# Kernel optimization log

Hardware: AMD Instinct MI355X
Metric: run time of the kernel (lower is better)

## Reference

```python
import jax, jax.numpy as jnp
import numpy as np

SCALE = 4.0
GRID = 64
B, T, A, C = 4, 256, 3, 13
F = 5 + C  # x,y,z,r,conf,cls...


def setup_inputs() -> dict:
    key = jax.random.key(0)
    k1, k2, k3, k4, k5 = jax.random.split(key, 5)
    p = jax.random.normal(k1, (B, A, GRID, GRID, GRID, F), dtype=jnp.float32)
    xyz = jax.random.uniform(k2, (B, T, 3), minval=4.0, maxval=SCALE * GRID - 4.0)
    r = jax.random.uniform(k3, (B, T, 1), minval=6.0, maxval=20.0)
    conf = (jax.random.uniform(k4, (B, T, 1)) < 0.6).astype(jnp.float32)
    cls = jax.nn.one_hot(jax.random.randint(k5, (B, T), 0, C), C, dtype=jnp.float32)
    targets = jnp.concatenate([xyz, r, conf, cls], axis=-1)  # [B,T,18]
    anchor = jnp.array([[[8.0], [12.0], [16.0]]], dtype=jnp.float32)  # [1,A,1]
    return {"p": p, "targets": targets, "anchor": anchor}


def _bce(logits, t):
    # BCEWithLogitsLoss (pos_weight=1), elementwise
    return t * jax.nn.softplus(-logits) + (1.0 - t) * jax.nn.softplus(logits)


def _eiou(box1, box2, eps=1e-7):
    # boxes are (x,y,z,r): axis-aligned cubes of side r centered at xyz (3D EIoU)
    c1, r1 = box1[:, :3], box1[:, 3]
    c2, r2 = box2[:, :3], box2[:, 3]
    h1, h2 = r1[:, None] * 0.5, r2[:, None] * 0.5
    lo = jnp.maximum(c1 - h1, c2 - h2)
    hi = jnp.minimum(c1 + h1, c2 + h2)
    inter = jnp.prod(jnp.clip(hi - lo, 0.0), axis=-1)
    union = r1 ** 3 + r2 ** 3 - inter + eps
    iou = inter / union
    clo = jnp.minimum(c1 - h1, c2 - h2)
    chi = jnp.maximum(c1 + h1, c2 + h2)
    cdim = chi - clo  # enclosing box per-axis extent
    rho2 = jnp.sum((c1 - c2) ** 2, axis=-1)
    c2diag = jnp.sum(cdim ** 2, axis=-1) + eps
    size_pen = jnp.sum(((r1 - r2) ** 2)[:, None] / (cdim ** 2 + eps), axis=-1)
    return iou - rho2 / c2diag - size_pen


def reference(p, targets, anchor):
    Bs, An, K, J, I, Fd = p.shape
    Cn = Fd - 5
    g, gr = 0.5, 0.0
    Tn = targets.shape[1]
    n = Bs * Tn
    x = targets.reshape(n, Fd)
    b0 = jnp.repeat(jnp.arange(Bs), Tn)
    conf_m = x[:, 4] > 0.5
    anchor_norm = anchor[0] / SCALE  # [A,1]
    gxyzr = x[:, :4] / SCALE
    rn = gxyzr[:, 3]
    ratio = rn[None, :] / anchor_norm  # [A,n]
    aok = jnp.maximum(ratio, 1.0 / ratio) < 4.0
    gxyz = gxyzr[:, :3]
    gdim = jnp.array([K, J, I], dtype=p.dtype)  # gain[1:]
    gxyz_i = gdim - gxyz
    m1 = (gxyz % 1.0 < g) & (gxyz > 1.0)
    m2 = (gxyz_i % 1.0 < g) & (gxyz_i > 1.0)
    fm = jnp.stack([jnp.ones_like(m1[:, 0]), m1[:, 0], m1[:, 1], m1[:, 2], m2[:, 0], m2[:, 1], m2[:, 2]])  # [7,n]
    off = jnp.array([[0, 0, 0], [1, 0, 0], [0, 1, 0], [0, 0, 1], [-1, 0, 0], [0, -1, 0], [0, 0, -1]], dtype=p.dtype) * g
    valid = (conf_m[None, None, :] & aok[None, :, :] & fm[:, None, :]).reshape(-1)  # [7*A*n]
    bidx = jnp.broadcast_to(b0[None, None, :], (7, An, n)).reshape(-1)
    aidx = jnp.broadcast_to(jnp.arange(An)[None, :, None], (7, An, n)).reshape(-1)
    gxyz_c = jnp.broadcast_to(gxyz[None, None], (7, An, n, 3))
    off_c = jnp.broadcast_to(off[:, None, None, :], (7, An, n, 3))
    gijk_f = jnp.trunc(jax.lax.stop_gradient(gxyz_c - off_c))  # torch .long() truncates
    gijk = gijk_f.astype(jnp.int32).reshape(-1, 3)
    gi = jnp.clip(gijk[:, 0], 0, I - 1)
    gj = jnp.clip(gijk[:, 1], 0, J - 1)
    gk = jnp.clip(gijk[:, 2], 0, K - 1)
    tbox = jnp.concatenate([(gxyz_c - gijk_f).reshape(-1, 3), jnp.broadcast_to(rn[None, None, :], (7, An, n)).reshape(-1, 1)], axis=1)
    anchors = anchor_norm[aidx]  # [N,1]
    tcls = jnp.broadcast_to(x[None, None, :, 5:], (7, An, n, Cn)).reshape(-1, Cn)
    pred = p[bidx, aidx, gk, gj, gi]  # [N,F]
    pxyz = jax.nn.sigmoid(pred[:, :3]) * 2.0 - 0.5
    pr = (jax.nn.sigmoid(pred[:, 3:4]) * 2.0) ** 2 * anchors
    pbox = jnp.concatenate([pxyz, pr], axis=1)
    ei = _eiou(pbox, tbox)
    w = valid.astype(p.dtype)
    nv = jnp.maximum(jnp.sum(w), 1.0)
    loss_bbox = jnp.sum(w * (1.0 - ei)) / nv  # masked mean == torch mean over filtered rows
    iou_d = jax.lax.stop_gradient(jnp.clip(ei, 0.0))
    objv = (1.0 - gr) + gr * iou_d  # gr=0 -> 1.0
    tobj = jnp.zeros((Bs, An, K, J, I), dtype=p.dtype).at[bidx, aidx, gk, gj, gi].max(w * objv)
    loss_cls = jnp.sum(w[:, None] * _bce(pred[:, 5:], tcls)) / (nv * Cn)
    loss_obj = jnp.mean(_bce(p[..., 4], tobj))
    lb = loss_bbox * 1.0
    lo = loss_obj * 20.0
    lc = loss_cls * 10.0
    return ((lb + lo + lc) * Bs, lo, lc)
```

## Files before the change

### kernel.cpp

```cpp
#include <hip/hip_runtime.h>
#include <math.h>

#define NTGT   1024
#define NCAND  (21 * NTGT)
#define NCELL  (4 * 3 * 64 * 64 * 64)
#define BITW   (NCELL / 32)

__device__ __forceinline__ float softplusf(float x) {
    return fmaxf(x, 0.0f) + log1pf(__expf(-fabsf(x)));
}
__device__ __forceinline__ float sigmoidf(float x) {
    return 1.0f / (1.0f + __expf(-x));
}

__global__ __launch_bounds__(256) void cand_kernel(
    const float* __restrict__ p, const float* __restrict__ tg,
    const float* __restrict__ anchor, float* __restrict__ acc,
    unsigned int* __restrict__ bitmap)
{
    int idx = blockIdx.x * 256 + threadIdx.x;
    float nv_v = 0.f, bb_v = 0.f, cl_v = 0.f;
    if (idx < NCAND) {
        int t  = idx & (NTGT - 1);
        int oa = idx >> 10;
        int a  = oa % 3;
        int o  = oa / 3;
        const float* x = tg + t * 18;
        float conf = x[4];
        float rn   = x[3] * 0.25f;
        float an   = anchor[a] * 0.25f;
        float ratio = rn / an;
        bool ok = (conf > 0.5f) && (fmaxf(ratio, 1.0f / ratio) < 4.0f);
        float gv[3] = { x[0] * 0.25f, x[1] * 0.25f, x[2] * 0.25f };
        float off[3] = { 0.f, 0.f, 0.f };
        if (o >= 1) {
            if (o <= 3) {
                int c = o - 1;
                float v = gv[c];
                ok = ok && ((v - floorf(v)) < 0.5f) && (v > 1.0f);
                off[c] = 0.5f;
            } else {
                int c = o - 4;
                float vi = 64.0f - gv[c];
                ok = ok && ((vi - floorf(vi)) < 0.5f) && (vi > 1.0f);
                off[c] = -0.5f;
            }
        }
        if (ok) {
            float tb[3]; int gq[3];
            #pragma unroll
            for (int c = 0; c < 3; c++) {
                float f = truncf(gv[c] - off[c]);
                tb[c] = gv[c] - f;
                int ii = (int)f;
                gq[c] = min(max(ii, 0), 63);
            }
            int b0 = t >> 8;
            unsigned int cell =
                ((((unsigned)(b0 * 3 + a) * 64u + (unsigned)gq[2]) * 64u
                  + (unsigned)gq[1]) * 64u) + (unsigned)gq[0];
            const float* pp = p + (size_t)cell * 18u;
            float pd[18];
            #pragma unroll
            for (int f = 0; f < 18; f++) pd[f] = pp[f];

            float c1[3];
            #pragma unroll
            for (int c = 0; c < 3; c++) c1[c] = sigmoidf(pd[c]) * 2.0f - 0.5f;
            float s4 = sigmoidf(pd[3]) * 2.0f;
            float r1 = s4 * s4 * an;
            float r2 = rn;

            float h1 = 0.5f * r1, h2 = 0.5f * r2;
            float inter = 1.f, rho2 = 0.f, c2d = 0.f, spen = 0.f;
            float dr2 = (r1 - r2) * (r1 - r2);
            #pragma unroll
            for (int c = 0; c < 3; c++) {
                float lo1 = c1[c] - h1, hi1 = c1[c] + h1;
                float lo2 = tb[c] - h2, hi2 = tb[c] + h2;
                inter *= fmaxf(fminf(hi1, hi2) - fmaxf(lo1, lo2), 0.f);
                float cd  = fmaxf(hi1, hi2) - fminf(lo1, lo2);
                float cd2 = cd * cd;
                float d   = c1[c] - tb[c];
                rho2 += d * d;
                c2d  += cd2;
                spen += dr2 / (cd2 + 1e-7f);
            }
            float uni = r1 * r1 * r1 + r2 * r2 * r2 - inter + 1e-7f;
            float ei  = inter / uni - rho2 / (c2d + 1e-7f) - spen;

            nv_v = 1.0f;
            bb_v = 1.0f - ei;
            float cl = 0.f;
            #pragma unroll
            for (int c = 0; c < 13; c++) {
                float l = pd[5 + c];
                cl += softplusf(l) - x[5 + c] * l;
            }
            cl_v = cl;
            atomicOr(&bitmap[cell >> 5], 1u << (cell & 31u));
        }
    }
    #pragma unroll
    for (int s = 32; s > 0; s >>= 1) {
        nv_v += __shfl_down(nv_v, s, 64);
        bb_v += __shfl_down(bb_v, s, 64);
        cl_v += __shfl_down(cl_v, s, 64);
    }
    if ((threadIdx.x & 63) == 0 && nv_v != 0.f) {
        atomicAdd(&acc[0], nv_v);
        atomicAdd(&acc[1], bb_v);
        atomicAdd(&acc[2], cl_v);
    }
}

__global__ __launch_bounds__(256) void obj_kernel(
    const float* __restrict__ p, const unsigned int* __restrict__ bitmap,
    float* __restrict__ acc)
{
    int stride = gridDim.x * blockDim.x;
    float s = 0.f;
    for (int i = blockIdx.x * blockDim.x + threadIdx.x; i < NCELL; i += stride) {
        float l = p[(size_t)i * 18u + 4u];
        unsigned int bit = (bitmap[i >> 5] >> (i & 31)) & 1u;
        s += softplusf(l) - (bit ? l : 0.f);
    }
    #pragma unroll
    for (int sh = 32; sh > 0; sh >>= 1) s += __shfl_down(s, sh, 64);
    __shared__ float sm[4];
    int lane = threadIdx.x & 63, w = threadIdx.x >> 6;
    if (lane == 0) sm[w] = s;
    __syncthreads();
    if (threadIdx.x == 0) {
        atomicAdd(&acc[3], sm[0] + sm[1] + sm[2] + sm[3]);
    }
}

__global__ void final_kernel(const float* __restrict__ acc, float* __restrict__ out)
{
    float nv = fmaxf(acc[0], 1.0f);
    float lb = acc[1] / nv;
    float lc = acc[2] / (nv * 13.0f) * 10.0f;
    float lo = acc[3] * (20.0f / (float)NCELL);
    out[0] = (lb + lo + lc) * 4.0f;
    out[1] = lo;
    out[2] = lc;
}

extern "C" void kernel_launch(void* const* d_in, const int* in_sizes, int n_in,
                              void* d_out, int out_size, void* d_ws, size_t ws_size,
                              hipStream_t stream) {
    const float* p       = (const float*)d_in[0];
    const float* targets = (const float*)d_in[1];
    const float* anchor  = (const float*)d_in[2];
    float* out = (float*)d_out;

    float* acc = (float*)d_ws;
    unsigned int* bitmap = (unsigned int*)((char*)d_ws + 16);

    hipMemsetAsync(d_ws, 0, 16 + (size_t)BITW * 4, stream);

    cand_kernel<<<NCAND / 256, 256, 0, stream>>>(p, targets, anchor, acc, bitmap);
    obj_kernel<<<3072, 256, 0, stream>>>(p, bitmap, acc);
    final_kernel<<<1, 1, 0, stream>>>(acc, out);
}
```

Measured before the change: 330.1 us.

## Fuse candidate and objectness kernels by subtracting unique positive logits

Measured after the change: 311.0 us. 1.06x faster.

```diff
diff --git a/kernel.cpp b/kernel.cpp
--- a/kernel.cpp
+++ b/kernel.cpp
@@ -3,127 +3,130 @@
 
 #define NTGT   1024
 #define NCAND  (21 * NTGT)
+#define NCBLK  (NCAND / 256)
 #define NCELL  (4 * 3 * 64 * 64 * 64)
 #define BITW   (NCELL / 32)
+#define NBLK   2048
 
 __device__ __forceinline__ float softplusf(float x) {
-    return fmaxf(x, 0.0f) + log1pf(__expf(-fabsf(x)));
+    return fmaxf(x, 0.0f) + __logf(1.0f + __expf(-fabsf(x)));
 }
 __device__ __forceinline__ float sigmoidf(float x) {
     return 1.0f / (1.0f + __expf(-x));
 }
 
-__global__ __launch_bounds__(256) void cand_kernel(
+__global__ __launch_bounds__(256) void fused_kernel(
     const float* __restrict__ p, const float* __restrict__ tg,
     const float* __restrict__ anchor, float* __restrict__ acc,
     unsigned int* __restrict__ bitmap)
 {
-    int idx = blockIdx.x * 256 + threadIdx.x;
-    float nv_v = 0.f, bb_v = 0.f, cl_v = 0.f;
-    if (idx < NCAND) {
-        int t  = idx & (NTGT - 1);
-        int oa = idx >> 10;
-        int a  = oa % 3;
-        int o  = oa / 3;
-        const float* x = tg + t * 18;
-        float conf = x[4];
-        float rn   = x[3] * 0.25f;
-        float an   = anchor[a] * 0.25f;
-        float ratio = rn / an;
-        bool ok = (conf > 0.5f) && (fmaxf(ratio, 1.0f / ratio) < 4.0f);
-        float gv[3] = { x[0] * 0.25f, x[1] * 0.25f, x[2] * 0.25f };
-        float off[3] = { 0.f, 0.f, 0.f };
-        if (o >= 1) {
-            if (o <= 3) {
-                int c = o - 1;
-                float v = gv[c];
-                ok = ok && ((v - floorf(v)) < 0.5f) && (v > 1.0f);
-                off[c] = 0.5f;
-            } else {
-                int c = o - 4;
-                float vi = 64.0f - gv[c];
-                ok = ok && ((vi - floorf(vi)) < 0.5f) && (vi > 1.0f);
-                off[c] = -0.5f;
+    if (blockIdx.x < NCBLK) {
+        int idx = blockIdx.x * 256 + threadIdx.x;
+        float nv_v = 0.f, bb_v = 0.f, cl_v = 0.f, ob_v = 0.f;
+        {
+            int t  = idx & (NTGT - 1);
+            int oa = idx >> 10;
+            int a  = oa % 3;
+            int o  = oa / 3;
+            const float* x = tg + t * 18;
+            float conf = x[4];
+            float rn   = x[3] * 0.25f;
+            float an   = anchor[a] * 0.25f;
+            float ratio = rn / an;
+            bool ok = (conf > 0.5f) && (fmaxf(ratio, 1.0f / ratio) < 4.0f);
+            float gv[3] = { x[0] * 0.25f, x[1] * 0.25f, x[2] * 0.25f };
+            float off[3] = { 0.f, 0.f, 0.f };
+            if (o >= 1) {
+                if (o <= 3) {
+                    int c = o - 1;
+                    float v = gv[c];
+                    ok = ok && ((v - floorf(v)) < 0.5f) && (v > 1.0f);
+                    off[c] = 0.5f;
+                } else {
+                    int c = o - 4;
+                    float vi = 64.0f - gv[c];
+                    ok = ok && ((vi - floorf(vi)) < 0.5f) && (vi > 1.0f);
+                    off[c] = -0.5f;
+                }
+            }
+            if (ok) {
+                float tb[3]; int gq[3];
+                #pragma unroll
+                for (int c = 0; c < 3; c++) {
+                    float f = truncf(gv[c] - off[c]);
+                    tb[c] = gv[c] - f;
+                    gq[c] = min(max((int)f, 0), 63);
+                }
+                int b0 = t >> 8;
+                unsigned int cell =
+                    ((((unsigned)(b0 * 3 + a) * 64u + (unsigned)gq[2]) * 64u
+                      + (unsigned)gq[1]) * 64u) + (unsigned)gq[0];
+                const float* pp = p + (size_t)cell * 18u;
+                float pd[18];
+                #pragma unroll
+                for (int f = 0; f < 18; f++) pd[f] = pp[f];
+
+                float c1[3];
+                #pragma unroll
+                for (int c = 0; c < 3; c++) c1[c] = sigmoidf(pd[c]) * 2.0f - 0.5f;
+                float s4 = sigmoidf(pd[3]) * 2.0f;
+                float r1 = s4 * s4 * an;
+                float r2 = rn;
+
+                float h1 = 0.5f * r1, h2 = 0.5f * r2;
+                float inter = 1.f, rho2 = 0.f, c2d = 0.f, spen = 0.f;
+                float dr2 = (r1 - r2) * (r1 - r2);
+                #pragma unroll
+                for (int c = 0; c < 3; c++) {
+                    float lo1 = c1[c] - h1, hi1 = c1[c] + h1;
+                    float lo2 = tb[c] - h2, hi2 = tb[c] + h2;
+                    inter *= fmaxf(fminf(hi1, hi2) - fmaxf(lo1, lo2), 0.f);
+                    float cd  = fmaxf(hi1, hi2) - fminf(lo1, lo2);
+                    float cd2 = cd * cd;
+                    float d   = c1[c] - tb[c];
+                    rho2 += d * d;
+                    c2d  += cd2;
+                    spen += dr2 / (cd2 + 1e-7f);
+                }
+                float uni = r1 * r1 * r1 + r2 * r2 * r2 - inter + 1e-7f;
+                float ei  = inter / uni - rho2 / (c2d + 1e-7f) - spen;
+
+                nv_v = 1.0f;
+                bb_v = 1.0f - ei;
+                float cl = 0.f;
+                #pragma unroll
+                for (int c = 0; c < 13; c++) {
+                    float l = pd[5 + c];
+                    cl += softplusf(l) - x[5 + c] * l;
+                }
+                cl_v = cl;
+                unsigned int old = atomicOr(&bitmap[cell >> 5], 1u << (cell & 31u));
+                if (!(old & (1u << (cell & 31u)))) ob_v = pd[4];
             }
         }
-        if (ok) {
-            float tb[3]; int gq[3];
-            #pragma unroll
-            for (int c = 0; c < 3; c++) {
-                float f = truncf(gv[c] - off[c]);
-                tb[c] = gv[c] - f;
-                int ii = (int)f;
-                gq[c] = min(max(ii, 0), 63);
-            }
-            int b0 = t >> 8;
-            unsigned int cell =
-                ((((unsigned)(b0 * 3 + a) * 64u + (unsigned)gq[2]) * 64u
-                  + (unsigned)gq[1]) * 64u) + (unsigned)gq[0];
-            const float* pp = p + (size_t)cell * 18u;
-            float pd[18];
-            #pragma unroll
-            for (int f = 0; f < 18; f++) pd[f] = pp[f];
-
-            float c1[3];
-            #pragma unroll
-            for (int c = 0; c < 3; c++) c1[c] = sigmoidf(pd[c]) * 2.0f - 0.5f;
-            float s4 = sigmoidf(pd[3]) * 2.0f;
-            float r1 = s4 * s4 * an;
-            float r2 = rn;
-
-            float h1 = 0.5f * r1, h2 = 0.5f * r2;
-            float inter = 1.f, rho2 = 0.f, c2d = 0.f, spen = 0.f;
-            float dr2 = (r1 - r2) * (r1 - r2);
-            #pragma unroll
-            for (int c = 0; c < 3; c++) {
-                float lo1 = c1[c] - h1, hi1 = c1[c] + h1;
-                float lo2 = tb[c] - h2, hi2 = tb[c] + h2;
-                inter *= fmaxf(fminf(hi1, hi2) - fmaxf(lo1, lo2), 0.f);
-                float cd  = fmaxf(hi1, hi2) - fminf(lo1, lo2);
-                float cd2 = cd * cd;
-                float d   = c1[c] - tb[c];
-                rho2 += d * d;
-                c2d  += cd2;
-                spen += dr2 / (cd2 + 1e-7f);
-            }
-            float uni = r1 * r1 * r1 + r2 * r2 * r2 - inter + 1e-7f;
-            float ei  = inter / uni - rho2 / (c2d + 1e-7f) - spen;
-
-            nv_v = 1.0f;
-            bb_v = 1.0f - ei;
-            float cl = 0.f;
-            #pragma unroll
-            for (int c = 0; c < 13; c++) {
-                float l = pd[5 + c];
-                cl += softplusf(l) - x[5 + c] * l;
-            }
-            cl_v = cl;
-            atomicOr(&bitmap[cell >> 5], 1u << (cell & 31u));
+        #pragma unroll
+        for (int s = 32; s > 0; s >>= 1) {
+            nv_v += __shfl_down(nv_v, s, 64);
+            bb_v += __shfl_down(bb_v, s, 64);
+            cl_v += __shfl_down(cl_v, s, 64);
+            ob_v += __shfl_down(ob_v, s, 64);
+        }
+        if ((threadIdx.x & 63) == 0 && nv_v != 0.f) {
+            atomicAdd(&acc[0], nv_v);
+            atomicAdd(&acc[1], bb_v);
+            atomicAdd(&acc[2], cl_v);
+            atomicAdd(&acc[4], ob_v);
         }
     }
-    #pragma unroll
-    for (int s = 32; s > 0; s >>= 1) {
-        nv_v += __shfl_down(nv_v, s, 64);
-        bb_v += __shfl_down(bb_v, s, 64);
-        cl_v += __shfl_down(cl_v, s, 64);
-    }
-    if ((threadIdx.x & 63) == 0 && nv_v != 0.f) {
-        atomicAdd(&acc[0], nv_v);
-        atomicAdd(&acc[1], bb_v);
-        atomicAdd(&acc[2], cl_v);
-    }
-}
 
-__global__ __launch_bounds__(256) void obj_kernel(
-    const float* __restrict__ p, const unsigned int* __restrict__ bitmap,
-    float* __restrict__ acc)
-{
-    int stride = gridDim.x * blockDim.x;
     float s = 0.f;
-    for (int i = blockIdx.x * blockDim.x + threadIdx.x; i < NCELL; i += stride) {
-        float l = p[(size_t)i * 18u + 4u];
-        unsigned int bit = (bitmap[i >> 5] >> (i & 31)) & 1u;
-        s += softplusf(l) - (bit ? l : 0.f);
+    {
+        int i = blockIdx.x * 256 + threadIdx.x;
+        #pragma unroll
+        for (int it = 0; it < NCELL / (NBLK * 256); it++) {
+            s += softplusf(p[(size_t)i * 18u + 4u]);
+            i += NBLK * 256;
+        }
     }
     #pragma unroll
     for (int sh = 32; sh > 0; sh >>= 1) s += __shfl_down(s, sh, 64);
@@ -141,7 +144,7 @@
     float nv = fmaxf(acc[0], 1.0f);
     float lb = acc[1] / nv;
     float lc = acc[2] / (nv * 13.0f) * 10.0f;
-    float lo = acc[3] * (20.0f / (float)NCELL);
+    float lo = (acc[3] - acc[4]) * (20.0f / (float)NCELL);
     out[0] = (lb + lo + lc) * 4.0f;
     out[1] = lo;
     out[2] = lc;
@@ -156,11 +159,10 @@
     float* out = (float*)d_out;
 
     float* acc = (float*)d_ws;
-    unsigned int* bitmap = (unsigned int*)((char*)d_ws + 16);
+    unsigned int* bitmap = (unsigned int*)((char*)d_ws + 32);
 
-    hipMemsetAsync(d_ws, 0, 16 + (size_t)BITW * 4, stream);
+    hipMemsetAsync(d_ws, 0, 32 + (size_t)BITW * 4, stream);
 
-    cand_kernel<<<NCAND / 256, 256, 0, stream>>>(p, targets, anchor, acc, bitmap);
-    obj_kernel<<<3072, 256, 0, stream>>>(p, bitmap, acc);
+    fused_kernel<<<NBLK, 256, 0, stream>>>(p, targets, anchor, acc, bitmap);
     final_kernel<<<1, 1, 0, stream>>>(acc, out);
 }
```
